# Optimization experiments

Hardware: AMD Instinct MI355X
Metric: run time of the kernel (lower is better)

The kernel has to match this reference:

```python
import jax, jax.numpy as jnp
import numpy as np
import math

BZ, SEQ, NV, VA, HA = 16, 5, 1, 8, 8
C, DSTATE, DCONV, EXPAND, NLAYER = 384, 16, 4, 2, 4
DI = EXPAND * C
DTR = math.ceil(C / 16)  # 24
NTOK = (NV + 2) * SEQ * VA * HA  # 960 multi-modal tokens
T = NTOK + 2                     # + 2 gps tokens


def _ln(x, g, b, eps=1e-5):
    m = jnp.mean(x, -1, keepdims=True)
    v = jnp.mean((x - m) ** 2, -1, keepdims=True)
    return (x - m) * jax.lax.rsqrt(v + eps) * g + b


def _mamba(x, in_w, cw, cb, xw, dtw, dtb, a_log, d, ow):
    # x: (B,T,C); Mamba with bias=False in/out proj, conv_bias=True (mamba_ssm defaults)
    xz = jnp.einsum('btc,ec->bte', x, in_w)            # (B,T,2*DI)
    xh, z = jnp.split(xz, 2, axis=-1)
    xt = jnp.swapaxes(xh, 1, 2)                        # (B,DI,T)
    xt = jax.lax.conv_general_dilated(
        xt, cw[:, None, :], (1,), [(DCONV - 1, 0)],
        feature_group_count=DI, dimension_numbers=('NCH', 'OIH', 'NCH'))
    xh = jax.nn.silu(jnp.swapaxes(xt, 1, 2) + cb)      # causal depthwise conv + SiLU
    xdbl = jnp.einsum('btd,ed->bte', xh, xw)           # (B,T,DTR+2*DS)
    dt, Bm, Cm = jnp.split(xdbl, [DTR, DTR + DSTATE], axis=-1)
    dt = jax.nn.softplus(jnp.einsum('btr,dr->btd', dt, dtw) + dtb)  # (B,T,DI)
    A = -jnp.exp(a_log)                                # (DI,DSTATE)

    def step(h, inp):
        dt_t, x_t, b_t, c_t = inp                      # (B,DI),(B,DI),(B,DS),(B,DS)
        h = h * jnp.exp(dt_t[..., None] * A) + (dt_t * x_t)[..., None] * b_t[:, None, :]
        return h, jnp.einsum('bds,bs->bd', h, c_t)

    h0 = jnp.zeros((x.shape[0], DI, DSTATE), x.dtype)
    xs = tuple(jnp.swapaxes(a, 0, 1) for a in (dt, xh, Bm, Cm))
    _, ys = jax.lax.scan(step, h0, xs)
    y = jnp.swapaxes(ys, 0, 1) + d * xh
    y = y * jax.nn.silu(z)
    return jnp.einsum('btd,cd->btc', y, ow)


def _forward(image_tensor, lidar_tensor, radar_tensor, gps, pos_emb,
             ln1_g, ln1_b, fc1_w, fc1_b, fc2_w, fc2_b,
             in_proj_w, conv_w, conv_b, x_proj_w, dt_proj_w, dt_proj_b,
             A_log, D_param, out_proj_w, ln_f_g, ln_f_b):
    bz = lidar_tensor.shape[0] // SEQ
    h, w = lidar_tensor.shape[2], lidar_tensor.shape[3]
    img = image_tensor.reshape(bz, NV * SEQ, -1, h, w)
    lid = lidar_tensor.reshape(bz, SEQ, -1, h, w)
    rad = radar_tensor.reshape(bz, SEQ, -1, h, w)
    s1, s2 = C // 3, C // 3 * 2
    cs_img = jnp.concatenate([img[:, :, :s1], lid[:, :, s1:s2], rad[:, :, s2:]], axis=2)
    cs_lid = jnp.concatenate([lid[:, :, :s1], rad[:, :, s1:s2], img[:, :, s2:]], axis=2)
    cs_rad = jnp.concatenate([rad[:, :, :s1], img[:, :, s1:s2], lid[:, :, s2:]], axis=2)
    tok = jnp.concatenate([cs_img, cs_lid, cs_rad], axis=1)     # (bz, 3*SEQ, C, h, w)
    tok = jnp.transpose(tok, (0, 1, 3, 4, 2)).reshape(bz, -1, C)
    tok = jnp.concatenate([tok, gps], axis=1)                   # (bz, T, C)
    x = pos_emb + tok                                           # dropout is identity (eval)
    for l in range(NLAYER):
        x_ln = _ln(x, ln1_g[l], ln1_b[l])
        x_fc1 = jnp.einsum('btc,ec->bte', x_ln, fc1_w[l]) + fc1_b[l]
        x_fm = _mamba(x_fc1, in_proj_w[l, 0], conv_w[l, 0], conv_b[l, 0],
                      x_proj_w[l, 0], dt_proj_w[l, 0], dt_proj_b[l, 0],
                      A_log[l, 0], D_param[l, 0], out_proj_w[l, 0])
        x_flip = jnp.flip(x_fc1, axis=1)
        x_bm = _mamba(x_flip, in_proj_w[l, 1], conv_w[l, 1], conv_b[l, 1],
                      x_proj_w[l, 1], dt_proj_w[l, 1], dt_proj_b[l, 1],
                      A_log[l, 1], D_param[l, 1], out_proj_w[l, 1])
        x_fc2 = jnp.einsum('btc,ec->bte', x_flip, fc2_w[l]) + fc2_b[l]
        x_relu = jnp.where(x_fc2 >= 0, x_fc2, 0.2 * x_fc2)      # LeakyReLU(0.2)
        x = x_bm * x_relu + x_fm * x_bm                         # note: x_bm stays flipped, as in original
    x = _ln(x, ln_f_g, ln_f_b)
    pos_out = x[:, NTOK:]
    x = x[:, :NTOK].reshape(bz, (NV + 2) * SEQ, VA, HA, C)
    x = jnp.transpose(x, (0, 1, 4, 2, 3))
    img_out = x[:, :NV * SEQ].reshape(bz * NV * SEQ, -1, h, w)
    lid_out = x[:, NV * SEQ:(NV + 1) * SEQ].reshape(bz * SEQ, -1, h, w)
    rad_out = x[:, (NV + 1) * SEQ:].reshape(bz * SEQ, -1, h, w)
    return img_out, lid_out, rad_out, pos_out


def setup_inputs() -> dict:
    key = jax.random.key(0)
    it = iter(jax.random.split(key, 24))

    def n(shape, s=0.02):
        return jax.random.normal(next(it), shape, jnp.float32) * s

    return dict(
        image_tensor=n((BZ * NV * SEQ, C, VA, HA), 1.0),
        lidar_tensor=n((BZ * SEQ, C, VA, HA), 1.0),
        radar_tensor=n((BZ * SEQ, C, VA, HA), 1.0),
        gps=n((BZ, 2, C), 1.0),
        pos_emb=n((1, T, C), 0.02),
        ln1_g=jnp.ones((NLAYER, C)), ln1_b=jnp.zeros((NLAYER, C)),
        fc1_w=n((NLAYER, C, C)), fc1_b=jnp.zeros((NLAYER, C)),
        fc2_w=n((NLAYER, C, C)), fc2_b=jnp.zeros((NLAYER, C)),
        in_proj_w=n((NLAYER, 2, 2 * DI, C)),
        conv_w=n((NLAYER, 2, DI, DCONV), 0.1),
        conv_b=jnp.zeros((NLAYER, 2, DI)),
        x_proj_w=n((NLAYER, 2, DTR + 2 * DSTATE, DI)),
        dt_proj_w=n((NLAYER, 2, DI, DTR), 0.1),
        dt_proj_b=jnp.full((NLAYER, 2, DI), -4.6, jnp.float32),  # softplus ~ 0.01
        A_log=jnp.tile(jnp.log(jnp.arange(1., DSTATE + 1, dtype=jnp.float32)), (NLAYER, 2, DI, 1)),
        D_param=jnp.ones((NLAYER, 2, DI)),
        out_proj_w=n((NLAYER, 2, C, DI)),
        ln_f_g=jnp.ones((C,)), ln_f_b=jnp.zeros((C,)),
    )


def reference(image_tensor, lidar_tensor, radar_tensor, gps, pos_emb,
              ln1_g, ln1_b, fc1_w, fc1_b, fc2_w, fc2_b,
              in_proj_w, conv_w, conv_b, x_proj_w, dt_proj_w, dt_proj_b,
              A_log, D_param, out_proj_w, ln_f_g, ln_f_b):
    return _forward(image_tensor, lidar_tensor, radar_tensor, gps, pos_emb,
                    ln1_g, ln1_b, fc1_w, fc1_b, fc2_w, fc2_b,
                    in_proj_w, conv_w, conv_b, x_proj_w, dt_proj_w, dt_proj_b,
                    A_log, D_param, out_proj_w, ln_f_g, ln_f_b)
```

## Files before the change

### kernel.cpp

```cpp
#include <hip/hip_runtime.h>
#include <cstdint>
#include <cstddef>


constexpr int BZv = 16, SEQ = 5, NV = 1;
constexpr int C = 384, DSTATE = 16, DCONV = 4, NLAYER = 4;
constexpr int DI = 768;
constexpr int DTR = 24;
constexpr int NTOK = (NV + 2) * SEQ * 64;
constexpr int T = NTOK + 2;
constexpr int M = BZv * T;
constexpr int HB = 8;
constexpr int MH = HB * T;
constexpr int XZdim = 2 * DI;
constexpr int ND = DTR + 2 * DSTATE;
constexpr int NDP = 32;
constexpr int NCHUNK = 26, TC = 37;
constexpr int NQ = 241;
constexpr size_t SEC_SZ = (size_t)BZv * SEQ * C * 64;

constexpr size_t SET1 = (size_t)C * C;
constexpr size_t SETI = (size_t)2 * DI * C;
constexpr size_t SETO = (size_t)C * DI;
constexpr size_t SETX = (size_t)64 * DI;
constexpr size_t SETD = (size_t)DI * 32;
constexpr size_t WSZ1 = 4 * SET1;
constexpr size_t WSZI = 8 * SETI;
constexpr size_t WSZO = 8 * SETO;
constexpr size_t WSZX = 8 * SETX;
constexpr size_t WSZD = 8 * SETD;

typedef __attribute__((ext_vector_type(8))) short short8;
typedef __attribute__((ext_vector_type(4))) float floatx4;

#define GLOAD_LDS16(g, l)                                        \
  __builtin_amdgcn_global_load_lds(                              \
      (const __attribute__((address_space(1))) void*)(g),        \
      (__attribute__((address_space(3))) void*)(l), 16, 0, 0)

__device__ __forceinline__ void split_bf16(float v, short& hi, short& lo) {
  unsigned u = __float_as_uint(v);
  unsigned hib = u & 0xFFFF0000u;
  float r = v - __uint_as_float(hib);
  hi = (short)(hib >> 16);
  lo = (short)(__float_as_uint(r) >> 16);
}

__device__ __forceinline__ float join_bf16(short h, short l) {
  return __uint_as_float((unsigned)(unsigned short)h << 16) +
         __uint_as_float((unsigned)(unsigned short)l << 16);
}

__device__ __forceinline__ void pow16(float e1, float* e) {
  e[0] = e1;
  e[1] = e1 * e1;
  e[3] = e[1] * e[1];
  e[7] = e[3] * e[3];
  e[15] = e[7] * e[7];
  e[2] = e[1] * e[0];
  e[4] = e[3] * e[0];
  e[5] = e[3] * e[1];
  e[6] = e[5] * e[0];
  e[8] = e[7] * e[0];
  e[9] = e[7] * e[1];
  e[10] = e[9] * e[0];
  e[11] = e[7] * e[3];
  e[12] = e[11] * e[0];
  e[13] = e[11] * e[1];
  e[14] = e[13] * e[0];
}

__global__ __launch_bounds__(256) void assemble_t_k(
    const float* __restrict__ img, const float* __restrict__ lid,
    const float* __restrict__ rad, const float* __restrict__ gps,
    const float* __restrict__ pe, float* __restrict__ x) {
  __shared__ float lds[64][129];
  int blk = blockIdx.x, tid = threadIdx.x;
  if (blk < 720) {
    int b = blk / 45;
    int rem = blk % 45;
    int g_ = rem / 3, cc = rem % 3;
    int sec = g_ / 5, s = g_ % 5;
    int srow = b * 5 + s;
    int which = (cc + sec) % 3;
    const float* src = (which == 0) ? img : (which == 1 ? lid : rad);
    const float* sp = src + (size_t)srow * (C * 64) + cc * 8192;
#pragma unroll
    for (int i = 0; i < 32; i++) {
      int lin = tid + 256 * i;
      lds[lin & 63][lin >> 6] = sp[lin];
    }
    __syncthreads();
#pragma unroll
    for (int i = 0; i < 32; i++) {
      int lin = tid + 256 * i;
      int p = lin >> 7, c = lin & 127;
      int t = g_ * 64 + p;
      int ccc = cc * 128 + c;
      x[((size_t)b * T + t) * C + ccc] = lds[p][c] + pe[(size_t)t * C + ccc];
    }
  } else {
#pragma unroll
    for (int i = 0; i < 48; i++) {
      int lin = tid + 256 * i;
      int r = lin / C, c = lin % C;
      int b = r >> 1, e = r & 1;
      x[((size_t)b * T + NTOK + e) * C + c] =
          gps[((size_t)b * 2 + e) * C + c] + pe[(size_t)(NTOK + e) * C + c];
    }
  }
}

__global__ __launch_bounds__(256) void ln_fused_k(
    const float* __restrict__ x, const float* __restrict__ g,
    const float* __restrict__ b, short* __restrict__ oh,
    short* __restrict__ ol) {
  int row = blockIdx.x * 4 + (threadIdx.x >> 6);
  int lane = threadIdx.x & 63;
  const float* xr = x + (size_t)row * C;
  float v[6];
  float s = 0.f;
#pragma unroll
  for (int j = 0; j < 6; j++) {
    v[j] = xr[lane + 64 * j];
    s += v[j];
  }
#pragma unroll
  for (int o = 32; o > 0; o >>= 1) s += __shfl_xor(s, o, 64);
  float mean = s * (1.f / 384.f);
  float q = 0.f;
#pragma unroll
  for (int j = 0; j < 6; j++) {
    float d = v[j] - mean;
    q += d * d;
  }
#pragma unroll
  for (int o = 32; o > 0; o >>= 1) q += __shfl_xor(q, o, 64);
  float rstd = rsqrtf(q * (1.f / 384.f) + 1e-5f);
#pragma unroll
  for (int j = 0; j < 6; j++) {
    int c = lane + 64 * j;
    float val = (v[j] - mean) * rstd * g[c] + b[c];
    short h, l;
    split_bf16(val, h, l);
    oh[(size_t)row * C + c] = h;
    ol[(size_t)row * C + c] = l;
  }
}

__global__ __launch_bounds__(256) void ln_stats2_k(const float* __restrict__ x,
                                                   float* __restrict__ stats) {
  int row = blockIdx.x * 4 + (threadIdx.x >> 6);
  int lane = threadIdx.x & 63;
  const float* xr = x + (size_t)row * C;
  float v[6];
  float s = 0.f;
#pragma unroll
  for (int j = 0; j < 6; j++) {
    v[j] = xr[lane + 64 * j];
    s += v[j];
  }
#pragma unroll
  for (int o = 32; o > 0; o >>= 1) s += __shfl_xor(s, o, 64);
  float mean = s * (1.f / 384.f);
  float q = 0.f;
#pragma unroll
  for (int j = 0; j < 6; j++) {
    float d = v[j] - mean;
    q += d * d;
  }
#pragma unroll
  for (int o = 32; o > 0; o >>= 1) q += __shfl_xor(q, o, 64);
  if (lane == 0) {
    stats[2 * row] = mean;
    stats[2 * row + 1] = rsqrtf(q * (1.f / 384.f) + 1e-5f);
  }
}

template <int NSRC, int KSRC, int KS>
__global__ __launch_bounds__(256) void cast_swz_k(const float* __restrict__ src,
                                                  short* __restrict__ oh,
                                                  short* __restrict__ ol) {
  constexpr int NP = (NSRC + 15) & ~15;
  constexpr size_t SETSZ = (size_t)NP * KS * 32;
  int set = blockIdx.y;
  size_t idx = (size_t)blockIdx.x * 256 + threadIdx.x;
  int e = (int)(idx & 7);
  int lane = (int)((idx >> 3) & 63);
  size_t rest = idx >> 9;
  int ks = (int)(rest % KS);
  int nf = (int)(rest / KS);
  int n = nf * 16 + (lane & 15);
  int k = ks * 32 + ((lane >> 4) << 3) + e;
  float v = 0.f;
  if (n < NSRC && k < KSRC)
    v = src[(size_t)set * NSRC * KSRC + (size_t)n * KSRC + k];
  short h, l;
  split_bf16(v, h, l);
  oh[(size_t)set * SETSZ + idx] = h;
  ol[(size_t)set * SETSZ + idx] = l;
}

template <int ACT, bool BIAS, bool FLIPA, bool OSPLIT, bool SWAPXY, bool XSWZ>
__global__ __launch_bounds__(256) void mgemm_k(
    const short* __restrict__ Ah, const short* __restrict__ Al, int K,
    const short* __restrict__ Wh, const short* __restrict__ Wl, int N,
    const float* __restrict__ bias, float* __restrict__ Co, int ldc,
    short* __restrict__ Oh, short* __restrict__ Ol, int Mrows, int arow_off,
    int crow_off, int nt, int mpx) {
  __shared__ __align__(16) short sAh[128 * 32];
  __shared__ __align__(16) short sAl[128 * 32];
  const int tid = threadIdx.x;
  const int wave = tid >> 6, lane = tid & 63;
  int bm_, bn_;
  if constexpr (XSWZ) {
    const int f = blockIdx.x;
    const int xcd = f & 7, j = f >> 3;
    bn_ = j % nt;
    bm_ = xcd * mpx + j / nt;
  } else {
    bm_ = SWAPXY ? blockIdx.x : blockIdx.y;
    bn_ = SWAPXY ? blockIdx.y : blockIdx.x;
  }
  const int m0 = bm_ * 128, n0 = bn_ * 128;
  const int lrow = lane >> 2, lchunk = lane & 3;
  const int wm = (wave >> 1) * 64, wn = (wave & 1) * 64;
  const int frow = lane & 15, fquad = lane >> 4;
  const int KST = K >> 5;
  const int nfb = (n0 + wn) >> 4;

  size_t arow[2];
#pragma unroll
  for (int p = 0; p < 2; p++) {
    int r = p * 64 + wave * 16 + lrow;
    int lm = m0 + r;
    if (lm >= Mrows) lm = Mrows - 1;
    int g = arow_off + lm;
    if (FLIPA) {
      int bb = g / T;
      int tt = g - bb * T;
      g = bb * T + (T - 1 - tt);
    }
    arow[p] = (size_t)g * K;
  }

  floatx4 acc[4][4] = {};
  for (int k0 = 0; k0 < K; k0 += 32) {
    if (k0) __syncthreads();
    const int kc = k0 + lchunk * 8;
#pragma unroll
    for (int p = 0; p < 2; p++) {
      GLOAD_LDS16(Ah + arow[p] + kc, &sAh[(p * 64 + wave * 16) * 32]);
      GLOAD_LDS16(Al + arow[p] + kc, &sAl[(p * 64 + wave * 16) * 32]);
    }
    const int ks = k0 >> 5;
    short8 bh[4], bl[4];
#pragma unroll
    for (int j = 0; j < 4; j++) {
      size_t bo = (((size_t)(nfb + j) * KST + ks) * 64 + lane) * 8;
      bh[j] = *(const short8*)&Wh[bo];
      bl[j] = *(const short8*)&Wl[bo];
    }
    __syncthreads();
    short8 ah[4], al[4];
#pragma unroll
    for (int i = 0; i < 4; i++) {
      int ra = (wm + i * 16 + frow) * 32 + fquad * 8;
      ah[i] = *(const short8*)&sAh[ra];
      al[i] = *(const short8*)&sAl[ra];
    }
#pragma unroll
    for (int i = 0; i < 4; i++)
#pragma unroll
      for (int j = 0; j < 4; j++) {
        acc[i][j] = __builtin_amdgcn_mfma_f32_16x16x32_bf16(ah[i], bh[j],
                                                            acc[i][j], 0, 0, 0);
        acc[i][j] = __builtin_amdgcn_mfma_f32_16x16x32_bf16(al[i], bh[j],
                                                            acc[i][j], 0, 0, 0);
        acc[i][j] = __builtin_amdgcn_mfma_f32_16x16x32_bf16(ah[i], bl[j],
                                                            acc[i][j], 0, 0, 0);
      }
  }
#pragma unroll
  for (int i = 0; i < 4; i++) {
#pragma unroll
    for (int r = 0; r < 4; r++) {
      int gm = m0 + wm + i * 16 + fquad * 4 + r;
      if (gm >= Mrows) continue;
      int grow = crow_off + gm;
#pragma unroll
      for (int j = 0; j < 4; j++) {
        int gn = n0 + wn + j * 16 + frow;
        if (gn >= N) continue;
        float v = acc[i][j][r];
        if constexpr (BIAS) v += bias[gn];
        if constexpr (ACT == 1) v = v >= 0.f ? v : 0.2f * v;
        if constexpr (OSPLIT) {
          short h, l;
          split_bf16(v, h, l);
          Oh[(size_t)grow * N + gn] = h;
          Ol[(size_t)grow * N + gn] = l;
        } else {
          Co[(size_t)grow * ldc + gn] = v;
        }
      }
    }
  }
}

template <int ACT, bool BIAS, int OMODE, int MT = 64, bool XSWZ = false>
__global__ __launch_bounds__(256) void mgemm64_k(
    const short* __restrict__ Ah, const short* __restrict__ Al, int lda, int K,
    const short* __restrict__ Wh, const short* __restrict__ Wl, int N,
    const float* __restrict__ bias, float* __restrict__ Co, int ldc,
    short* __restrict__ Oh, short* __restrict__ Ol,
    const float* __restrict__ e1, const float* __restrict__ e2, int Mrows,
    int crow_off, int nt, int mpx) {
  __shared__ __align__(16) short sAh[MT * 32];
  __shared__ __align__(16) short sAl[MT * 32];
  const int tid = threadIdx.x;
  const int wave = tid >> 6, lane = tid & 63;
  int bm_, bn_;
  if constexpr (XSWZ) {
    const int f = blockIdx.x;
    const int xcd = f & 7, j = f >> 3;
    bn_ = j % nt;
    bm_ = xcd * mpx + j / nt;
  } else {
    bm_ = blockIdx.y;
    bn_ = blockIdx.x;
  }
  const int m0 = bm_ * MT, n0 = bn_ * 64;
  const int schunk = tid & 3;
  const int frow = lane & 15, fquad = lane >> 4;
  const int KST = K >> 5;
  const int nfw = (n0 >> 4) + wave;

  int lm = m0 + ((MT == 64) ? (tid >> 2) : (lane >> 2));
  if (lm >= Mrows) lm = Mrows - 1;
  size_t aoff = (size_t)lm * lda;

  floatx4 acc[MT / 16] = {};
  for (int k0 = 0; k0 < K; k0 += 32) {
    if (k0) __syncthreads();
    const int kc = k0 + schunk * 8;
    if constexpr (MT == 64) {
      GLOAD_LDS16(Ah + aoff + kc, &sAh[(wave * 16) * 32]);
      GLOAD_LDS16(Al + aoff + kc, &sAl[(wave * 16) * 32]);
    } else {
      if (wave == 0) GLOAD_LDS16(Ah + aoff + kc, &sAh[0]);
      if (wave == 1) GLOAD_LDS16(Al + aoff + kc, &sAl[0]);
    }
    const int ks = k0 >> 5;
    short8 bh, bl;
    {
      size_t bo = (((size_t)nfw * KST + ks) * 64 + lane) * 8;
      bh = *(const short8*)&Wh[bo];
      bl = *(const short8*)&Wl[bo];
    }
    __syncthreads();
    short8 ah[MT / 16], al[MT / 16];
#pragma unroll
    for (int i = 0; i < MT / 16; i++) {
      int ra = (i * 16 + frow) * 32 + fquad * 8;
      ah[i] = *(const short8*)&sAh[ra];
      al[i] = *(const short8*)&sAl[ra];
    }
#pragma unroll
    for (int i = 0; i < MT / 16; i++) {
      acc[i] = __builtin_amdgcn_mfma_f32_16x16x32_bf16(ah[i], bh, acc[i], 0, 0, 0);
      acc[i] = __builtin_amdgcn_mfma_f32_16x16x32_bf16(al[i], bh, acc[i], 0, 0, 0);
      acc[i] = __builtin_amdgcn_mfma_f32_16x16x32_bf16(ah[i], bl, acc[i], 0, 0, 0);
    }
  }
  const int gn = n0 + wave * 16 + frow;
  if (gn < N) {
#pragma unroll
    for (int i = 0; i < MT / 16; i++) {
#pragma unroll
      for (int r = 0; r < 4; r++) {
        int gm = m0 + i * 16 + fquad * 4 + r;
        if (gm >= Mrows) continue;
        int grow = crow_off + gm;
        float v = acc[i][r];
        if constexpr (BIAS) v += bias[gn];
        if constexpr (ACT == 2) v = (v > 20.f) ? v : __logf(1.f + __expf(v));
        if constexpr (ACT == 4) {
          size_t o = (size_t)grow * ldc + gn;
          v = e2[o] * (e1[o] + v);
        }
        if constexpr (OMODE == 2) {
          if (gn < NDP) {
            short h, l;
            split_bf16(v, h, l);
            Oh[(size_t)grow * NDP + gn] = h;
            Ol[(size_t)grow * NDP + gn] = l;
          }
          if (gn >= DTR) Co[(size_t)grow * 32 + (gn - DTR)] = v;
        } else {
          Co[(size_t)grow * ldc + gn] = v;
        }
      }
    }
  }
}

__global__ __launch_bounds__(256) void conv_k(const float* __restrict__ xz,
                                              const float* __restrict__ cw,
                                              const float* __restrict__ cb,
                                              short* __restrict__ xch,
                                              short* __restrict__ xcl) {
  int idx = blockIdx.x * 256 + threadIdx.x;
  int dh = idx % (DI / 2);
  int rem = idx / (DI / 2);
  int q = rem % NQ;
  int b = rem / NQ;
  int d = dh * 2;
  int t0 = q * 4;
  const float* base = xz + (size_t)b * T * XZdim + d;
  float4 cwa = *(const float4*)&cw[d * 4];
  float4 cwb = *(const float4*)&cw[(d + 1) * 4];
  float cb0 = cb[d], cb1 = cb[d + 1];
  float2 w[7];
#pragma unroll
  for (int j = 0; j < 7; j++) {
    int tt = t0 - 3 + j;
    w[j] = (tt >= 0 && tt < T) ? *(const float2*)(base + (size_t)tt * XZdim)
                               : make_float2(0.f, 0.f);
  }
  const float cwx[4] = {cwa.x, cwa.y, cwa.z, cwa.w};
  const float cwy[4] = {cwb.x, cwb.y, cwb.z, cwb.w};
#pragma unroll
  for (int r = 0; r < 4; r++) {
    int t = t0 + r;
    if (t >= T) break;
    float a0 = cb0, a1 = cb1;
#pragma unroll
    for (int j = 0; j < 4; j++) {
      a0 += w[r + j].x * cwx[j];
      a1 += w[r + j].y * cwy[j];
    }
    float v0 = a0 / (1.f + __expf(-a0));
    float v1 = a1 / (1.f + __expf(-a1));
    short h0, l0, h1, l1;
    split_bf16(v0, h0, l0);
    split_bf16(v1, h1, l1);
    size_t o = ((size_t)b * T + t) * DI + d;
    *(short2*)&xch[o] = make_short2(h0, h1);
    *(short2*)&xcl[o] = make_short2(l0, l1);
  }
}

__global__ __launch_bounds__(256) void scan_p1_k(
    const float* __restrict__ xzb, const short* __restrict__ xch,
    const short* __restrict__ xcl, const float* __restrict__ xdbc,
    const float* __restrict__ alog, float* __restrict__ hchk,
    float* __restrict__ sdt) {
  int d = blockIdx.x * 256 + threadIdx.x;
  int ch = blockIdx.y, b = blockIdx.z;
  float A[DSTATE], h[DSTATE];
  bool powA = true;
#pragma unroll
  for (int s = 0; s < DSTATE; s++) {
    A[s] = -expf(alog[d * DSTATE + s]);
    powA = powA && (fabsf(A[s] + (float)(s + 1)) <= 1e-4f * (float)(s + 1));
    h[s] = 0.f;
  }
  const int t0 = ch * TC;
  const float* xzr = xzb + ((size_t)b * T + t0) * XZdim;
  const short* xchr = xch + ((size_t)b * T + t0) * DI;
  const short* xclr = xcl + ((size_t)b * T + t0) * DI;
  const float* bcr = xdbc + ((size_t)b * T + t0) * 32;
  float sd = 0.f;
  if (powA) {
    for (int t = 0; t < TC; t++) {
      float dt = xzr[(size_t)t * XZdim + d];
      float xv = join_bf16(xchr[(size_t)t * DI + d], xclr[(size_t)t * DI + d]);
      float dx = dt * xv;
      const float* bc = bcr + (size_t)t * 32;
      sd += dt;
      float ev[DSTATE];
      pow16(__expf(-dt), ev);
#pragma unroll
      for (int s = 0; s < DSTATE; s++) h[s] = h[s] * ev[s] + dx * bc[s];
    }
  } else {
    for (int t = 0; t < TC; t++) {
      float dt = xzr[(size_t)t * XZdim + d];
      float xv = join_bf16(xchr[(size_t)t * DI + d], xclr[(size_t)t * DI + d]);
      float dx = dt * xv;
      const float* bc = bcr + (size_t)t * 32;
      sd += dt;
#pragma unroll
      for (int s = 0; s < DSTATE; s++)
        h[s] = h[s] * __expf(dt * A[s]) + dx * bc[s];
    }
  }
  size_t o = ((size_t)(b * NCHUNK + ch) * DSTATE) * DI + d;
#pragma unroll
  for (int s = 0; s < DSTATE; s++) hchk[o + (size_t)s * DI] = h[s];
  sdt[(size_t)(b * NCHUNK + ch) * DI + d] = sd;
}

__global__ __launch_bounds__(256) void scan_p2_k(float* __restrict__ hchk,
                                                 const float* __restrict__ sdt,
                                                 const float* __restrict__ alog) {
  int idx = blockIdx.x * 256 + threadIdx.x;
  int d = idx % DI;
  int rem = idx / DI;
  int s = rem % DSTATE, b = rem / DSTATE;
  float A = -expf(alog[d * DSTATE + s]);
  float hin = 0.f;
#pragma unroll
  for (int ch = 0; ch < NCHUNK; ch++) {
    size_t o = ((size_t)(b * NCHUNK + ch) * DSTATE + s) * DI + d;
    float P = __expf(A * sdt[(size_t)(b * NCHUNK + ch) * DI + d]);
    float hl = hchk[o];
    hchk[o] = hin;
    hin = P * hin + hl;
  }
}

__global__ __launch_bounds__(256) void scan_p3_k(
    const float* __restrict__ xzb, const short* __restrict__ xch,
    const short* __restrict__ xcl, const float* __restrict__ xdbc,
    const float* __restrict__ alog, const float* __restrict__ Dp,
    const float* __restrict__ hchk, short* __restrict__ yh,
    short* __restrict__ yl) {
  int d = blockIdx.x * 256 + threadIdx.x;
  int ch = blockIdx.y, b = blockIdx.z;
  float A[DSTATE], h[DSTATE];
  bool powA = true;
  size_t o = ((size_t)(b * NCHUNK + ch) * DSTATE) * DI + d;
#pragma unroll
  for (int s = 0; s < DSTATE; s++) {
    A[s] = -expf(alog[d * DSTATE + s]);
    powA = powA && (fabsf(A[s] + (float)(s + 1)) <= 1e-4f * (float)(s + 1));
    h[s] = hchk[o + (size_t)s * DI];
  }
  float Dd = Dp[d];
  const int t0 = ch * TC;
  const float* xzr = xzb + ((size_t)b * T + t0) * XZdim;
  const short* xchr = xch + ((size_t)b * T + t0) * DI;
  const short* xclr = xcl + ((size_t)b * T + t0) * DI;
  const float* bcr = xdbc + ((size_t)b * T + t0) * 32;
  if (powA) {
    for (int t = 0; t < TC; t++) {
      float dt = xzr[(size_t)t * XZdim + d];
      float xv = join_bf16(xchr[(size_t)t * DI + d], xclr[(size_t)t * DI + d]);
      float zv = xzr[(size_t)t * XZdim + DI + d];
      float dx = dt * xv;
      float accv = 0.f;
      const float* bc = bcr + (size_t)t * 32;
      float ev[DSTATE];
      pow16(__expf(-dt), ev);
#pragma unroll
      for (int s = 0; s < DSTATE; s++) {
        h[s] = h[s] * ev[s] + dx * bc[s];
        accv += h[s] * bc[DSTATE + s];
      }
      float y = accv + Dd * xv;
      float sz = zv / (1.f + __expf(-zv));
      float v = y * sz;
      short hh, ll;
      split_bf16(v, hh, ll);
      size_t oi = ((size_t)(b * T + t0 + t)) * DI + d;
      yh[oi] = hh;
      yl[oi] = ll;
    }
  } else {
    for (int t = 0; t < TC; t++) {
      float dt = xzr[(size_t)t * XZdim + d];
      float xv = join_bf16(xchr[(size_t)t * DI + d], xclr[(size_t)t * DI + d]);
      float zv = xzr[(size_t)t * XZdim + DI + d];
      float dx = dt * xv;
      float accv = 0.f;
      const float* bc = bcr + (size_t)t * 32;
#pragma unroll
      for (int s = 0; s < DSTATE; s++) {
        h[s] = h[s] * __expf(dt * A[s]) + dx * bc[s];
        accv += h[s] * bc[DSTATE + s];
      }
      float y = accv + Dd * xv;
      float sz = zv / (1.f + __expf(-zv));
      float v = y * sz;
      short hh, ll;
      split_bf16(v, hh, ll);
      size_t oi = ((size_t)(b * T + t0 + t)) * DI + d;
      yh[oi] = hh;
      yl[oi] = ll;
    }
  }
}

__global__ __launch_bounds__(256) void ln_scatter_k(
    const float* __restrict__ x, const float* __restrict__ stats,
    const float* __restrict__ g, const float* __restrict__ bb,
    float* __restrict__ out) {
  __shared__ float lds[64][129];
  int blk = blockIdx.x, tid = threadIdx.x;
  if (blk < 240) {
    int b = blk / 15, g_ = blk % 15;
    int sec = g_ / 5, s = g_ % 5;
    const int rbase = b * T + g_ * 64;
    for (int cc = 0; cc < 3; cc++) {
      if (cc) __syncthreads();
#pragma unroll
      for (int i = 0; i < 32; i++) {
        int lin = tid + 256 * i;
        int p = lin >> 7, c = lin & 127;
        int row = rbase + p;
        int ccc = cc * 128 + c;
        float v = x[(size_t)row * C + ccc];
        v = (v - stats[2 * row]) * stats[2 * row + 1] * g[ccc] + bb[ccc];
        lds[p][c] = v;
      }
      __syncthreads();
      size_t obase = (size_t)sec * SEC_SZ +
                     (((size_t)(b * 5 + s) * C + cc * 128) << 6);
#pragma unroll
      for (int i = 0; i < 32; i++) {
        int lin = tid + 256 * i;
        int c = lin >> 6, p = lin & 63;
        out[obase + ((size_t)c << 6) + p] = lds[p][c];
      }
    }
  } else {
#pragma unroll
    for (int i = 0; i < 48; i++) {
      int lin = tid + 256 * i;
      int r = lin / C, c = lin % C;
      int b = r >> 1, e = r & 1;
      int row = b * T + NTOK + e;
      float v = x[(size_t)row * C + c];
      v = (v - stats[2 * row]) * stats[2 * row + 1] * g[c] + bb[c];
      out[3 * SEC_SZ + ((size_t)(b * 2 + e)) * C + c] = v;
    }
  }
}

extern "C" void kernel_launch(void* const* d_in, const int* in_sizes, int n_in,
                              void* d_out, int out_size, void* d_ws,
                              size_t ws_size, hipStream_t stream) {
  const float* image = (const float*)d_in[0];
  const float* lidar = (const float*)d_in[1];
  const float* radar = (const float*)d_in[2];
  const float* gps = (const float*)d_in[3];
  const float* pe = (const float*)d_in[4];
  const float* ln1g = (const float*)d_in[5];
  const float* ln1b = (const float*)d_in[6];
  const float* fc1w = (const float*)d_in[7];
  const float* fc1b = (const float*)d_in[8];
  const float* fc2w = (const float*)d_in[9];
  const float* fc2b_ = (const float*)d_in[10];
  const float* inw = (const float*)d_in[11];
  const float* cw = (const float*)d_in[12];
  const float* cb = (const float*)d_in[13];
  const float* xw = (const float*)d_in[14];
  const float* dtw = (const float*)d_in[15];
  const float* dtb = (const float*)d_in[16];
  const float* alog = (const float*)d_in[17];
  const float* Dp = (const float*)d_in[18];
  const float* ow = (const float*)d_in[19];
  const float* lnfg = (const float*)d_in[20];
  const float* lnfb = (const float*)d_in[21];
  float* out = (float*)d_out;

  constexpr size_t MC = (size_t)M * C;
  float* ws = (float*)d_ws;
  float* x = ws;
  float* fcb = x + MC;
  float* bmfm = fcb + MC;
  float* x1f = bmfm + MC;
  float* yf = x1f + MC;
  float* xz_h = yf + MC;
  float* xcp = xz_h + (size_t)MH * XZdim;
  float* xdp = xcp + (size_t)MH * DI;
  float* wpl = xdp + (size_t)MH * 64;

  constexpr size_t CHK_H = (size_t)HB * NCHUNK * DSTATE * DI;
  static_assert(CHK_H + (size_t)HB * NCHUNK * DI <= MC / 2, "alias overflow");
  float* hchk = x + MC / 2;
  float* sdtb = hchk + CHK_H;

  short* lnh = (short*)bmfm;
  short* lnl = lnh + MC;
  float* bm = bmfm;
  short* x1h = (short*)x1f;
  short* x1l = x1h + MC;
  short* yh = (short*)yf;
  short* yl = yh + (size_t)MH * DI;
  short* xch = (short*)xcp;
  short* xcl = xch + (size_t)MH * DI;
  short* xdh = (short*)xdp;
  short* xdl = xdh + (size_t)MH * NDP;
  float* xdbc = xdp + (size_t)MH * 32;

  short* wf1h = (short*)wpl;
  short* wf1l = wf1h + WSZ1;
  short* wf2h = wf1l + WSZ1;
  short* wf2l = wf2h + WSZ1;
  short* winh = wf2l + WSZ1;
  short* winl = winh + WSZI;
  short* wowh = winl + WSZI;
  short* wowl = wowh + WSZO;
  short* wxh = wowl + WSZO;
  short* wxl = wxh + WSZX;
  short* wdth = wxl + WSZX;
  short* wdtl = wdth + WSZD;
  float* stats2 = (float*)(wdtl + WSZD);

  cast_swz_k<C, C, 12><<<dim3((int)(SET1 / 256), 4), 256, 0, stream>>>(
      fc1w, wf1h, wf1l);
  cast_swz_k<C, C, 12><<<dim3((int)(SET1 / 256), 4), 256, 0, stream>>>(
      fc2w, wf2h, wf2l);
  cast_swz_k<2 * DI, C, 12><<<dim3((int)(SETI / 256), 8), 256, 0, stream>>>(
      inw, winh, winl);
  cast_swz_k<C, DI, 24><<<dim3((int)(SETO / 256), 8), 256, 0, stream>>>(
      ow, wowh, wowl);
  cast_swz_k<ND, DI, 24><<<dim3((int)(SETX / 256), 8), 256, 0, stream>>>(
      xw, wxh, wxl);
  cast_swz_k<DI, DTR, 1><<<dim3((int)(SETD / 256), 8), 256, 0, stream>>>(
      dtw, wdth, wdtl);

  assemble_t_k<<<721, 256, 0, stream>>>(image, lidar, radar, gps, pe, x);

  for (int l = 0; l < NLAYER; l++) {
    ln_fused_k<<<M / 4, 256, 0, stream>>>(x, ln1g + l * C, ln1b + l * C, lnh,
                                          lnl);
    mgemm_k<0, true, false, true, false, true><<<384, 256, 0, stream>>>(
        lnh, lnl, C, wf1h + l * SET1, wf1l + l * SET1, C, fc1b + l * C,
        nullptr, 0, x1h, x1l, M, 0, 0, 3, 16);
    mgemm_k<1, true, true, false, false, true><<<384, 256, 0, stream>>>(
        x1h, x1l, C, wf2h + l * SET1, wf2l + l * SET1, C, fc2b_ + l * C, fcb,
        C, nullptr, nullptr, M, 0, 0, 3, 16);
    for (int di = 0; di < 2; di++) {
      const int dir = 1 - di;
      size_t wo = (size_t)(l * 2 + dir);
      for (int h = 0; h < 2; h++) {
        const int roff = h * MH;
        if (dir == 0)
          mgemm_k<0, false, false, false, false, true><<<768, 256, 0, stream>>>(
              x1h, x1l, C, winh + wo * SETI, winl + wo * SETI, 2 * DI, nullptr,
              xz_h, XZdim, nullptr, nullptr, MH, roff, 0, 12, 8);
        else
          mgemm_k<0, false, true, false, false, true><<<768, 256, 0, stream>>>(
              x1h, x1l, C, winh + wo * SETI, winl + wo * SETI, 2 * DI, nullptr,
              xz_h, XZdim, nullptr, nullptr, MH, roff, 0, 12, 8);
        conv_k<<<(HB * NQ * (DI / 2)) / 256, 256, 0, stream>>>(
            xz_h, cw + wo * DI * DCONV, cb + wo * DI, xch, xcl);
        mgemm64_k<0, false, 2, 16><<<dim3(1, MH / 16), 256, 0, stream>>>(
            xch, xcl, DI, DI, wxh + wo * SETX, wxl + wo * SETX, ND, nullptr,
            xdbc, 0, xdh, xdl, nullptr, nullptr, MH, 0, 0, 0);
        mgemm64_k<2, true, 0><<<dim3(12, 121), 256, 0, stream>>>(
            xdh, xdl, NDP, 32, wdth + wo * SETD, wdtl + wo * SETD, DI,
            dtb + wo * DI, xz_h, XZdim, nullptr, nullptr, nullptr, nullptr,
            MH, 0, 0, 0);
        scan_p1_k<<<dim3(3, NCHUNK, HB), 256, 0, stream>>>(
            xz_h, xch, xcl, xdbc, alog + wo * DI * DSTATE, hchk, sdtb);
        scan_p2_k<<<(HB * DSTATE * DI) / 256, 256, 0, stream>>>(
            hchk, sdtb, alog + wo * DI * DSTATE);
        scan_p3_k<<<dim3(3, NCHUNK, HB), 256, 0, stream>>>(
            xz_h, xch, xcl, xdbc, alog + wo * DI * DSTATE, Dp + wo * DI, hchk,
            yh, yl);
        if (dir == 1)
          mgemm64_k<0, false, 0, 64, true><<<768, 256, 0, stream>>>(
              yh, yl, DI, DI, wowh + wo * SETO, wowl + wo * SETO, C, nullptr,
              bm, C, nullptr, nullptr, nullptr, nullptr, MH, roff, 6, 16);
        else
          mgemm64_k<4, false, 0, 64, true><<<768, 256, 0, stream>>>(
              yh, yl, DI, DI, wowh + wo * SETO, wowl + wo * SETO, C, nullptr,
              x, C, nullptr, nullptr, fcb, bm, MH, roff, 6, 16);
      }
    }
  }
  ln_stats2_k<<<M / 4, 256, 0, stream>>>(x, stats2);
  ln_scatter_k<<<241, 256, 0, stream>>>(x, stats2, lnfg, lnfb, out);
}
```

Before: 2.891 ms.

## Fuse dt projection and softplus into scan kernels; widen conv time tile

Removes the separate dt_proj GEMM, which wrote a softplus(dt) tensor into the xz buffer, and its weight cast. Both scan passes now compute dt per timestep from the 24 dt-rank values of x_proj output, using dt_proj weights staged in shared memory, so the intermediate write and reread go away. x_proj output is now stored as plain fp32 at stride 64. The dt math is done twice (p1 and p3) in exchange for one less launch and less traffic. Separately, the conv kernel now handles 8 timesteps per thread instead of 4, which cuts redundant halo loads.

```diff
diff --git a/kernel.cpp b/kernel.cpp
--- a/kernel.cpp
+++ b/kernel.cpp
@@ -14,21 +14,18 @@
 constexpr int MH = HB * T;
 constexpr int XZdim = 2 * DI;
 constexpr int ND = DTR + 2 * DSTATE;
-constexpr int NDP = 32;
 constexpr int NCHUNK = 26, TC = 37;
-constexpr int NQ = 241;
+constexpr int NQ8 = 121;
 constexpr size_t SEC_SZ = (size_t)BZv * SEQ * C * 64;
 
 constexpr size_t SET1 = (size_t)C * C;
 constexpr size_t SETI = (size_t)2 * DI * C;
 constexpr size_t SETO = (size_t)C * DI;
 constexpr size_t SETX = (size_t)64 * DI;
-constexpr size_t SETD = (size_t)DI * 32;
 constexpr size_t WSZ1 = 4 * SET1;
 constexpr size_t WSZI = 8 * SETI;
 constexpr size_t WSZO = 8 * SETO;
 constexpr size_t WSZX = 8 * SETX;
-constexpr size_t WSZD = 8 * SETD;
 
 typedef __attribute__((ext_vector_type(8))) short short8;
 typedef __attribute__((ext_vector_type(4))) float floatx4;
@@ -308,12 +305,11 @@
   }
 }
 
-template <int ACT, bool BIAS, int OMODE, int MT = 64, bool XSWZ = false>
+template <int ACT, bool BIAS, int MT = 64, bool XSWZ = false>
 __global__ __launch_bounds__(256) void mgemm64_k(
     const short* __restrict__ Ah, const short* __restrict__ Al, int lda, int K,
     const short* __restrict__ Wh, const short* __restrict__ Wl, int N,
     const float* __restrict__ bias, float* __restrict__ Co, int ldc,
-    short* __restrict__ Oh, short* __restrict__ Ol,
     const float* __restrict__ e1, const float* __restrict__ e2, int Mrows,
     int crow_off, int nt, int mpx) {
   __shared__ __align__(16) short sAh[MT * 32];
@@ -384,22 +380,11 @@
         int grow = crow_off + gm;
         float v = acc[i][r];
         if constexpr (BIAS) v += bias[gn];
-        if constexpr (ACT == 2) v = (v > 20.f) ? v : __logf(1.f + __expf(v));
         if constexpr (ACT == 4) {
           size_t o = (size_t)grow * ldc + gn;
           v = e2[o] * (e1[o] + v);
         }
-        if constexpr (OMODE == 2) {
-          if (gn < NDP) {
-            short h, l;
-            split_bf16(v, h, l);
-            Oh[(size_t)grow * NDP + gn] = h;
-            Ol[(size_t)grow * NDP + gn] = l;
-          }
-          if (gn >= DTR) Co[(size_t)grow * 32 + (gn - DTR)] = v;
-        } else {
-          Co[(size_t)grow * ldc + gn] = v;
-        }
+        Co[(size_t)grow * ldc + gn] = v;
       }
     }
   }
@@ -413,17 +398,17 @@
   int idx = blockIdx.x * 256 + threadIdx.x;
   int dh = idx % (DI / 2);
   int rem = idx / (DI / 2);
-  int q = rem % NQ;
-  int b = rem / NQ;
+  int q = rem % NQ8;
+  int b = rem / NQ8;
   int d = dh * 2;
-  int t0 = q * 4;
+  int t0 = q * 8;
   const float* base = xz + (size_t)b * T * XZdim + d;
   float4 cwa = *(const float4*)&cw[d * 4];
   float4 cwb = *(const float4*)&cw[(d + 1) * 4];
   float cb0 = cb[d], cb1 = cb[d + 1];
-  float2 w[7];
-#pragma unroll
-  for (int j = 0; j < 7; j++) {
+  float2 w[11];
+#pragma unroll
+  for (int j = 0; j < 11; j++) {
     int tt = t0 - 3 + j;
     w[j] = (tt >= 0 && tt < T) ? *(const float2*)(base + (size_t)tt * XZdim)
                                : make_float2(0.f, 0.f);
@@ -431,7 +416,7 @@
   const float cwx[4] = {cwa.x, cwa.y, cwa.z, cwa.w};
   const float cwy[4] = {cwb.x, cwb.y, cwb.z, cwb.w};
 #pragma unroll
-  for (int r = 0; r < 4; r++) {
+  for (int r = 0; r < 8; r++) {
     int t = t0 + r;
     if (t >= T) break;
     float a0 = cb0, a1 = cb1;
@@ -451,13 +436,24 @@
   }
 }
 
+
 __global__ __launch_bounds__(256) void scan_p1_k(
-    const float* __restrict__ xzb, const short* __restrict__ xch,
-    const short* __restrict__ xcl, const float* __restrict__ xdbc,
-    const float* __restrict__ alog, float* __restrict__ hchk,
-    float* __restrict__ sdt) {
-  int d = blockIdx.x * 256 + threadIdx.x;
+    const short* __restrict__ xch, const short* __restrict__ xcl,
+    const float* __restrict__ xdbc, const float* __restrict__ dtw,
+    const float* __restrict__ dtb, const float* __restrict__ alog,
+    float* __restrict__ hchk, float* __restrict__ sdt) {
+  __shared__ float sw[256][25];
+  __shared__ float sb[256];
+  int tid = threadIdx.x;
+  int d = blockIdx.x * 256 + tid;
   int ch = blockIdx.y, b = blockIdx.z;
+  {
+    const float* src = dtw + (size_t)blockIdx.x * 256 * DTR;
+    for (int idx = tid; idx < 256 * DTR; idx += 256)
+      sw[idx / DTR][idx % DTR] = src[idx];
+    sb[tid] = dtb[d];
+  }
+  __syncthreads();
   float A[DSTATE], h[DSTATE];
   bool powA = true;
 #pragma unroll
@@ -467,33 +463,38 @@
     h[s] = 0.f;
   }
   const int t0 = ch * TC;
-  const float* xzr = xzb + ((size_t)b * T + t0) * XZdim;
   const short* xchr = xch + ((size_t)b * T + t0) * DI;
   const short* xclr = xcl + ((size_t)b * T + t0) * DI;
-  const float* bcr = xdbc + ((size_t)b * T + t0) * 32;
+  const float* bcr = xdbc + ((size_t)b * T + t0) * 64;
   float sd = 0.f;
   if (powA) {
     for (int t = 0; t < TC; t++) {
-      float dt = xzr[(size_t)t * XZdim + d];
+      const float* bc = bcr + (size_t)t * 64;
+      float a = sb[tid];
+#pragma unroll
+      for (int j = 0; j < DTR; j++) a = fmaf(bc[j], sw[tid][j], a);
+      float dt = (a > 20.f) ? a : __logf(1.f + __expf(a));
       float xv = join_bf16(xchr[(size_t)t * DI + d], xclr[(size_t)t * DI + d]);
       float dx = dt * xv;
-      const float* bc = bcr + (size_t)t * 32;
       sd += dt;
       float ev[DSTATE];
       pow16(__expf(-dt), ev);
 #pragma unroll
-      for (int s = 0; s < DSTATE; s++) h[s] = h[s] * ev[s] + dx * bc[s];
+      for (int s = 0; s < DSTATE; s++) h[s] = h[s] * ev[s] + dx * bc[24 + s];
     }
   } else {
     for (int t = 0; t < TC; t++) {
-      float dt = xzr[(size_t)t * XZdim + d];
+      const float* bc = bcr + (size_t)t * 64;
+      float a = sb[tid];
+#pragma unroll
+      for (int j = 0; j < DTR; j++) a = fmaf(bc[j], sw[tid][j], a);
+      float dt = (a > 20.f) ? a : __logf(1.f + __expf(a));
       float xv = join_bf16(xchr[(size_t)t * DI + d], xclr[(size_t)t * DI + d]);
       float dx = dt * xv;
-      const float* bc = bcr + (size_t)t * 32;
       sd += dt;
 #pragma unroll
       for (int s = 0; s < DSTATE; s++)
-        h[s] = h[s] * __expf(dt * A[s]) + dx * bc[s];
+        h[s] = h[s] * __expf(dt * A[s]) + dx * bc[24 + s];
     }
   }
   size_t o = ((size_t)(b * NCHUNK + ch) * DSTATE) * DI + d;
@@ -524,11 +525,22 @@
 __global__ __launch_bounds__(256) void scan_p3_k(
     const float* __restrict__ xzb, const short* __restrict__ xch,
     const short* __restrict__ xcl, const float* __restrict__ xdbc,
+    const float* __restrict__ dtw, const float* __restrict__ dtb,
     const float* __restrict__ alog, const float* __restrict__ Dp,
     const float* __restrict__ hchk, short* __restrict__ yh,
     short* __restrict__ yl) {
-  int d = blockIdx.x * 256 + threadIdx.x;
+  __shared__ float sw[256][25];
+  __shared__ float sb[256];
+  int tid = threadIdx.x;
+  int d = blockIdx.x * 256 + tid;
   int ch = blockIdx.y, b = blockIdx.z;
+  {
+    const float* src = dtw + (size_t)blockIdx.x * 256 * DTR;
+    for (int idx = tid; idx < 256 * DTR; idx += 256)
+      sw[idx / DTR][idx % DTR] = src[idx];
+    sb[tid] = dtb[d];
+  }
+  __syncthreads();
   float A[DSTATE], h[DSTATE];
   bool powA = true;
   size_t o = ((size_t)(b * NCHUNK + ch) * DSTATE) * DI + d;
@@ -543,21 +555,24 @@
   const float* xzr = xzb + ((size_t)b * T + t0) * XZdim;
   const short* xchr = xch + ((size_t)b * T + t0) * DI;
   const short* xclr = xcl + ((size_t)b * T + t0) * DI;
-  const float* bcr = xdbc + ((size_t)b * T + t0) * 32;
+  const float* bcr = xdbc + ((size_t)b * T + t0) * 64;
   if (powA) {
     for (int t = 0; t < TC; t++) {
-      float dt = xzr[(size_t)t * XZdim + d];
+      const float* bc = bcr + (size_t)t * 64;
+      float a = sb[tid];
+#pragma unroll
+      for (int j = 0; j < DTR; j++) a = fmaf(bc[j], sw[tid][j], a);
+      float dt = (a > 20.f) ? a : __logf(1.f + __expf(a));
       float xv = join_bf16(xchr[(size_t)t * DI + d], xclr[(size_t)t * DI + d]);
       float zv = xzr[(size_t)t * XZdim + DI + d];
       float dx = dt * xv;
       float accv = 0.f;
-      const float* bc = bcr + (size_t)t * 32;
       float ev[DSTATE];
       pow16(__expf(-dt), ev);
 #pragma unroll
       for (int s = 0; s < DSTATE; s++) {
-        h[s] = h[s] * ev[s] + dx * bc[s];
-        accv += h[s] * bc[DSTATE + s];
+        h[s] = h[s] * ev[s] + dx * bc[24 + s];
+        accv += h[s] * bc[40 + s];
       }
       float y = accv + Dd * xv;
       float sz = zv / (1.f + __expf(-zv));
@@ -570,16 +585,19 @@
     }
   } else {
     for (int t = 0; t < TC; t++) {
-      float dt = xzr[(size_t)t * XZdim + d];
+      const float* bc = bcr + (size_t)t * 64;
+      float a = sb[tid];
+#pragma unroll
+      for (int j = 0; j < DTR; j++) a = fmaf(bc[j], sw[tid][j], a);
+      float dt = (a > 20.f) ? a : __logf(1.f + __expf(a));
       float xv = join_bf16(xchr[(size_t)t * DI + d], xclr[(size_t)t * DI + d]);
       float zv = xzr[(size_t)t * XZdim + DI + d];
       float dx = dt * xv;
       float accv = 0.f;
-      const float* bc = bcr + (size_t)t * 32;
 #pragma unroll
       for (int s = 0; s < DSTATE; s++) {
-        h[s] = h[s] * __expf(dt * A[s]) + dx * bc[s];
-        accv += h[s] * bc[DSTATE + s];
+        h[s] = h[s] * __expf(dt * A[s]) + dx * bc[24 + s];
+        accv += h[s] * bc[40 + s];
       }
       float y = accv + Dd * xv;
       float sz = zv / (1.f + __expf(-zv));
@@ -675,8 +693,8 @@
   float* yf = x1f + MC;
   float* xz_h = yf + MC;
   float* xcp = xz_h + (size_t)MH * XZdim;
-  float* xdp = xcp + (size_t)MH * DI;
-  float* wpl = xdp + (size_t)MH * 64;
+  float* xdbc = xcp + (size_t)MH * DI;
+  float* wpl = xdbc + (size_t)MH * 64;
 
   constexpr size_t CHK_H = (size_t)HB * NCHUNK * DSTATE * DI;
   static_assert(CHK_H + (size_t)HB * NCHUNK * DI <= MC / 2, "alias overflow");
@@ -692,9 +710,6 @@
   short* yl = yh + (size_t)MH * DI;
   short* xch = (short*)xcp;
   short* xcl = xch + (size_t)MH * DI;
-  short* xdh = (short*)xdp;
-  short* xdl = xdh + (size_t)MH * NDP;
-  float* xdbc = xdp + (size_t)MH * 32;
 
   short* wf1h = (short*)wpl;
   short* wf1l = wf1h + WSZ1;
@@ -706,9 +721,7 @@
   short* wowl = wowh + WSZO;
   short* wxh = wowl + WSZO;
   short* wxl = wxh + WSZX;
-  short* wdth = wxl + WSZX;
-  short* wdtl = wdth + WSZD;
-  float* stats2 = (float*)(wdtl + WSZD);
+  float* stats2 = (float*)(wxl + WSZX);
 
   cast_swz_k<C, C, 12><<<dim3((int)(SET1 / 256), 4), 256, 0, stream>>>(
       fc1w, wf1h, wf1l);
@@ -720,8 +733,6 @@
       ow, wowh, wowl);
   cast_swz_k<ND, DI, 24><<<dim3((int)(SETX / 256), 8), 256, 0, stream>>>(
       xw, wxh, wxl);
-  cast_swz_k<DI, DTR, 1><<<dim3((int)(SETD / 256), 8), 256, 0, stream>>>(
-      dtw, wdth, wdtl);
 
   assemble_t_k<<<721, 256, 0, stream>>>(image, lidar, radar, gps, pe, x);
 
@@ -747,30 +758,27 @@
           mgemm_k<0, false, true, false, false, true><<<768, 256, 0, stream>>>(
               x1h, x1l, C, winh + wo * SETI, winl + wo * SETI, 2 * DI, nullptr,
               xz_h, XZdim, nullptr, nullptr, MH, roff, 0, 12, 8);
-        conv_k<<<(HB * NQ * (DI / 2)) / 256, 256, 0, stream>>>(
+        conv_k<<<(HB * NQ8 * (DI / 2)) / 256, 256, 0, stream>>>(
             xz_h, cw + wo * DI * DCONV, cb + wo * DI, xch, xcl);
-        mgemm64_k<0, false, 2, 16><<<dim3(1, MH / 16), 256, 0, stream>>>(
+        mgemm64_k<0, false, 16><<<dim3(1, MH / 16), 256, 0, stream>>>(
             xch, xcl, DI, DI, wxh + wo * SETX, wxl + wo * SETX, ND, nullptr,
-            xdbc, 0, xdh, xdl, nullptr, nullptr, MH, 0, 0, 0);
-        mgemm64_k<2, true, 0><<<dim3(12, 121), 256, 0, stream>>>(
-            xdh, xdl, NDP, 32, wdth + wo * SETD, wdtl + wo * SETD, DI,
-            dtb + wo * DI, xz_h, XZdim, nullptr, nullptr, nullptr, nullptr,
-            MH, 0, 0, 0);
+            xdbc, 64, nullptr, nullptr, MH, 0, 0, 0);
         scan_p1_k<<<dim3(3, NCHUNK, HB), 256, 0, stream>>>(
-            xz_h, xch, xcl, xdbc, alog + wo * DI * DSTATE, hchk, sdtb);
+            xch, xcl, xdbc, dtw + wo * DI * DTR, dtb + wo * DI,
+            alog + wo * DI * DSTATE, hchk, sdtb);
         scan_p2_k<<<(HB * DSTATE * DI) / 256, 256, 0, stream>>>(
             hchk, sdtb, alog + wo * DI * DSTATE);
         scan_p3_k<<<dim3(3, NCHUNK, HB), 256, 0, stream>>>(
-            xz_h, xch, xcl, xdbc, alog + wo * DI * DSTATE, Dp + wo * DI, hchk,
-            yh, yl);
+            xz_h, xch, xcl, xdbc, dtw + wo * DI * DTR, dtb + wo * DI,
+            alog + wo * DI * DSTATE, Dp + wo * DI, hchk, yh, yl);
         if (dir == 1)
-          mgemm64_k<0, false, 0, 64, true><<<768, 256, 0, stream>>>(
+          mgemm64_k<0, false, 64, true><<<768, 256, 0, stream>>>(
               yh, yl, DI, DI, wowh + wo * SETO, wowl + wo * SETO, C, nullptr,
-              bm, C, nullptr, nullptr, nullptr, nullptr, MH, roff, 6, 16);
+              bm, C, nullptr, nullptr, MH, roff, 6, 16);
         else
-          mgemm64_k<4, false, 0, 64, true><<<768, 256, 0, stream>>>(
+          mgemm64_k<4, false, 64, true><<<768, 256, 0, stream>>>(
               yh, yl, DI, DI, wowh + wo * SETO, wowl + wo * SETO, C, nullptr,
-              x, C, nullptr, nullptr, fcb, bm, MH, roff, 6, 16);
+              x, C, fcb, bm, MH, roff, 6, 16);
       }
     }
   }
```

New measurement: 2.972 ms. +2.8%, slower.
